# Optimization experiments

Hardware: AMD Instinct MI355X
Metric: run time of the kernel (lower is better)

The kernel has to match this reference:

```python
import jax, jax.numpy as jnp
import numpy as np

B, C, H, W = 8, 256, 64, 64
NH = 8            # num_heads
OC = 256          # out_channels
D = C // NH       # per-head channel dim = 32
HW = H * W
BN_EPS = 1e-5


def _conv1x1(x, Wt, b):
    # x: [B,Cin,H,W], Wt: [Cout,Cin]
    return jnp.einsum('bchw,oc->bohw', x, Wt) + b[None, :, None, None]


def setup_inputs() -> dict:
    key = jax.random.key(0)
    ks = jax.random.split(key, 16)
    def n(k, shape, s=0.05):
        return jax.random.normal(k, shape, dtype=jnp.float32) * s
    return {
        'F1': jax.random.normal(ks[0], (B, C, H, W), jnp.float32),
        'F2': jax.random.normal(ks[1], (B, C, H, W), jnp.float32),
        'Wq':  n(ks[2], (C, 2 * C)), 'bq':  n(ks[3], (C,)),
        'Wk1': n(ks[4], (C, C)),     'bk1': n(ks[5], (C,)),
        'Wv1': n(ks[6], (C, C)),     'bv1': n(ks[7], (C,)),
        'Wk2': n(ks[8], (C, C)),     'bk2': n(ks[9], (C,)),
        'Wv2': n(ks[10], (C, C)),    'bv2': n(ks[11], (C,)),
        'mu':  jnp.full((1,), 0.5, jnp.float32),   # learnable scalar (init 0 in torch; nonzero here for nontrivial math)
        'Wc':  n(ks[12], (OC, 2 * C, 3, 3)),
        'gamma': jnp.ones((OC,), jnp.float32),
        'beta':  jnp.zeros((OC,), jnp.float32),
        'rmean': jnp.zeros((OC,), jnp.float32),
        'rvar':  jnp.ones((OC,), jnp.float32),
    }


def reference(F1, F2, Wq, bq, Wk1, bk1, Wv1, bv1, Wk2, bk2, Wv2, bv2,
              mu, Wc, gamma, beta, rmean, rvar):
    # fused query from both streams
    Qf = _conv1x1(jnp.concatenate([F1, F2], axis=1), Wq, bq)          # [B,C,H,W]
    Q = Qf.reshape(B, NH, D, HW).transpose(0, 1, 3, 2)                # [B,h,HW,d]
    Qs = jax.nn.softmax(Q, axis=-1)                                   # softmax over d

    def branch(F, Wk, bk, Wv, bv):
        K = _conv1x1(F, Wk, bk).reshape(B, NH, D, HW)                 # [B,h,d,HW]
        V = _conv1x1(F, Wv, bv).reshape(B, NH, D, HW)                 # [B,h,d,HW]
        Ks = jax.nn.softmax(K, axis=-1)                               # softmax over HW
        Att = jnp.einsum('bhdn,bhne->bhde', Ks, Qs)                   # [B,h,d,d]
        Xw = jnp.einsum('bhde,bhen->bhdn', Att, V)                    # [B,h,d,HW]
        return Xw.reshape(B, C, H, W)

    X1 = branch(F1, Wk1, bk1, Wv1, bv1)
    X2 = branch(F2, Wk2, bk2, Wv2, bv2)

    fused = jnp.concatenate([mu * X1 + F1, mu * X2 + F2], axis=1)     # [B,2C,H,W]
    y = jax.lax.conv_general_dilated(
        fused, Wc, window_strides=(1, 1), padding='SAME',
        dimension_numbers=('NCHW', 'OIHW', 'NCHW'))                   # [B,OC,H,W]
    # inference-mode BatchNorm + ReLU
    inv = gamma / jnp.sqrt(rvar + BN_EPS)
    y = y * inv[None, :, None, None] + (beta - rmean * inv)[None, :, None, None]
    return jax.nn.relu(y)
```

## Files before the change

### kernel.cpp

```cpp
#include <hip/hip_runtime.h>

typedef __attribute__((ext_vector_type(8))) short bf8;
typedef __attribute__((ext_vector_type(4))) float f32x4;

static __device__ __forceinline__ unsigned short f2b(float x) {
    unsigned u = __builtin_bit_cast(unsigned, x);
    u += 0x7fffu + ((u >> 16) & 1u);
    return (unsigned short)(u >> 16);
}

static __device__ __forceinline__ void gload_lds16(const void* g, void* l) {
    __builtin_amdgcn_global_load_lds(
        (const __attribute__((address_space(1))) unsigned int*)g,
        (__attribute__((address_space(3))) unsigned int*)l, 16, 0, 0);
}

__global__ __launch_bounds__(256) void k_prep_w(
    const float* __restrict__ Wq, const float* __restrict__ Wk1, const float* __restrict__ Wv1,
    const float* __restrict__ Wk2, const float* __restrict__ Wv2, const float* __restrict__ Wc,
    const float* __restrict__ gamma, const float* __restrict__ beta,
    const float* __restrict__ rmean, const float* __restrict__ rvar,
    unsigned short* __restrict__ WQB, unsigned short* __restrict__ WK1B, unsigned short* __restrict__ WV1B,
    unsigned short* __restrict__ WK2B, unsigned short* __restrict__ WV2B, unsigned short* __restrict__ WCB,
    float* __restrict__ BNS, float* __restrict__ BNB)
{
    const int total = 131072 + 4 * 65536 + 1179648 + 256;
    for (int i = blockIdx.x * blockDim.x + threadIdx.x; i < total; i += gridDim.x * blockDim.x) {
        int j = i;
        if (j < 131072) { WQB[j] = f2b(Wq[j]); continue; }
        j -= 131072;
        if (j < 65536) { WK1B[j] = f2b(Wk1[j]); continue; }
        j -= 65536;
        if (j < 65536) { WV1B[j] = f2b(Wv1[j]); continue; }
        j -= 65536;
        if (j < 65536) { WK2B[j] = f2b(Wk2[j]); continue; }
        j -= 65536;
        if (j < 65536) { WV2B[j] = f2b(Wv2[j]); continue; }
        j -= 65536;
        if (j < 1179648) {
            int cl = j & 63;
            int rest = j >> 6;
            int o = rest & 255;
            int tc = rest >> 8;
            int tap = tc >> 3, ccb = tc & 7;
            int c = ccb * 64 + cl;
            WCB[j] = f2b(Wc[(size_t)(o * 512 + c) * 9 + tap]);
            continue;
        }
        j -= 1179648;
        float inv = gamma[j] * rsqrtf(rvar[j] + 1e-5f);
        BNS[j] = inv;
        BNB[j] = beta[j] - rmean[j] * inv;
    }
}

__global__ __launch_bounds__(256) void k_xt(const float* __restrict__ F1, const float* __restrict__ F2,
                                            unsigned short* __restrict__ XT)
{
    __shared__ float tile[64][65];
    const int b = blockIdx.z;
    const int c0 = blockIdx.y * 64;
    const int p0 = blockIdx.x * 64;
    const int tx = threadIdx.x & 63;
    const int ty = threadIdx.x >> 6;
    const float* src = (c0 < 256) ? F1 : F2;
    const int cb = c0 & 255;
#pragma unroll
    for (int i = 0; i < 16; i++) {
        int cl = i * 4 + ty;
        tile[cl][tx] = src[((size_t)b * 256 + cb + cl) * 4096 + p0 + tx];
    }
    __syncthreads();
    const int t = threadIdx.x;
    const int p = t >> 2;
    const int cg = (t & 3) * 16;
    unsigned short tmp[16];
#pragma unroll
    for (int j = 0; j < 16; j++) tmp[j] = f2b(tile[cg + j][p]);
    unsigned short* dst = XT + ((size_t)b * 4096 + p0 + p) * 512 + c0 + cg;
    *(uint4*)dst = *(const uint4*)tmp;
    *(uint4*)(dst + 8) = *(const uint4*)(tmp + 8);
}

template<int MODE>
__global__ __launch_bounds__(256) void k_gemm1x1(
    const unsigned short* __restrict__ A,
    const unsigned short* __restrict__ XT,
    const float* __restrict__ bias,
    unsigned short* __restrict__ outU,
    float* __restrict__ outF,
    const unsigned short* __restrict__ QSp,
    float* __restrict__ ATTP,
    int Kd, int coff)
{
    __shared__ unsigned short lds[2][2][128 * 64];
    const int b = blockIdx.z;
    const int m0 = blockIdx.y * 128;
    const int n0 = blockIdx.x * 128;
    const int lane = threadIdx.x & 63;
    const int wv = threadIdx.x >> 6;
    const int wr = wv >> 1, wc = wv & 1;
    const int lrow = lane & 15, kg = lane >> 4;
    const int px = lane >> 3, sl = lane & 7;
    const int nt = Kd >> 6;

    f32x4 acc[4][4];
#pragma unroll
    for (int mi = 0; mi < 4; mi++)
#pragma unroll
        for (int ni = 0; ni < 4; ni++)
            acc[mi][ni] = (f32x4){0.f, 0.f, 0.f, 0.f};

#pragma unroll
    for (int j = 0; j < 4; j++) {
        int r0 = wv * 32 + j * 8;
        gload_lds16(A + (size_t)(m0 + r0 + px) * Kd + (sl ^ px) * 8, &lds[0][0][r0 * 64]);
        gload_lds16(XT + ((size_t)b * 4096 + n0 + r0 + px) * 512 + coff + (sl ^ px) * 8, &lds[0][1][r0 * 64]);
    }
    __syncthreads();

    int cb = 0;
    for (int kt = 0; kt < nt; kt++) {
        if (kt + 1 < nt) {
            int k0 = (kt + 1) << 6;
            int nb = cb ^ 1;
#pragma unroll
            for (int j = 0; j < 4; j++) {
                int r0 = wv * 32 + j * 8;
                gload_lds16(A + (size_t)(m0 + r0 + px) * Kd + k0 + (sl ^ px) * 8, &lds[nb][0][r0 * 64]);
                gload_lds16(XT + ((size_t)b * 4096 + n0 + r0 + px) * 512 + coff + k0 + (sl ^ px) * 8, &lds[nb][1][r0 * 64]);
            }
        }
        const unsigned short* wa = lds[cb][0];
        const unsigned short* wb = lds[cb][1];
#pragma unroll
        for (int klo = 0; klo < 64; klo += 32) {
            const int slin = klo >> 3;
            bf8 a[4], bv[4];
#pragma unroll
            for (int mi = 0; mi < 4; mi++) {
                int ol = wr * 64 + mi * 16 + lrow;
                a[mi] = *(const bf8*)(wa + ol * 64 + (((slin + kg) ^ (ol & 7)) * 8));
            }
#pragma unroll
            for (int ni = 0; ni < 4; ni++) {
                int nl = wc * 64 + ni * 16 + lrow;
                bv[ni] = *(const bf8*)(wb + nl * 64 + (((slin + kg) ^ (nl & 7)) * 8));
            }
#pragma unroll
            for (int mi = 0; mi < 4; mi++)
#pragma unroll
                for (int ni = 0; ni < 4; ni++)
                    acc[mi][ni] = __builtin_amdgcn_mfma_f32_16x16x32_bf16(a[mi], bv[ni], acc[mi][ni], 0, 0, 0);
        }
        __syncthreads();
        cb ^= 1;
    }

    if (MODE == 1) {
#pragma unroll
        for (int mi = 0; mi < 4; mi++) {
#pragma unroll
            for (int ni = 0; ni < 4; ni++) {
                int row0 = m0 + wr * 64 + mi * 16 + kg * 4;
                int col = n0 + wc * 64 + ni * 16 + lrow;
                int h = row0 >> 5, e0 = row0 & 31;
                unsigned long long pk = 0;
#pragma unroll
                for (int r = 0; r < 4; r++) {
                    unsigned short us = f2b(acc[mi][ni][r] + bias[row0 + r]);
                    pk |= (unsigned long long)us << (16 * r);
                }
                *(unsigned long long*)(outU + (((size_t)b * 8 + h) * 4096 + col) * 32 + e0) = pk;
            }
        }
    } else if (MODE == 2) {
#pragma unroll
        for (int hh = 0; hh < 2; hh++) {
            float vv[2][4][4];
            float mx[4];
#pragma unroll
            for (int ni = 0; ni < 4; ni++) mx[ni] = -1e30f;
#pragma unroll
            for (int ms = 0; ms < 2; ms++) {
                int mi = hh * 2 + ms;
                int row0 = m0 + wr * 64 + mi * 16 + kg * 4;
#pragma unroll
                for (int r = 0; r < 4; r++) {
                    float bi = bias[row0 + r];
#pragma unroll
                    for (int ni = 0; ni < 4; ni++) {
                        float x = acc[mi][ni][r] + bi;
                        vv[ms][r][ni] = x;
                        mx[ni] = fmaxf(mx[ni], x);
                    }
                }
            }
#pragma unroll
            for (int ni = 0; ni < 4; ni++) {
                mx[ni] = fmaxf(mx[ni], __shfl_xor(mx[ni], 16, 64));
                mx[ni] = fmaxf(mx[ni], __shfl_xor(mx[ni], 32, 64));
            }
            float sm[4] = {0.f, 0.f, 0.f, 0.f};
#pragma unroll
            for (int ms = 0; ms < 2; ms++)
#pragma unroll
                for (int r = 0; r < 4; r++)
#pragma unroll
                    for (int ni = 0; ni < 4; ni++) {
                        float e = __expf(vv[ms][r][ni] - mx[ni]);
                        vv[ms][r][ni] = e;
                        sm[ni] += e;
                    }
#pragma unroll
            for (int ni = 0; ni < 4; ni++) {
                sm[ni] += __shfl_xor(sm[ni], 16, 64);
                sm[ni] += __shfl_xor(sm[ni], 32, 64);
                sm[ni] = 1.0f / sm[ni];
            }
            int h = (m0 + wr * 64 + hh * 32) >> 5;
#pragma unroll
            for (int ms = 0; ms < 2; ms++) {
                int e0 = ms * 16 + kg * 4;
#pragma unroll
                for (int r = 0; r < 4; r++)
#pragma unroll
                    for (int ni = 0; ni < 4; ni++) {
                        int col = n0 + wc * 64 + ni * 16 + lrow;
                        outU[((size_t)(b * 8 + h) * 32 + e0 + r) * 4096 + col] = f2b(vv[ms][r][ni] * sm[ni]);
                    }
            }
        }
    } else {
        unsigned short* P = &lds[0][0][0];
        float* red = (float*)&lds[1][0][0];
        float ps[4][4];
#pragma unroll
        for (int mi = 0; mi < 4; mi++) {
            int rowl0 = wr * 64 + mi * 16 + kg * 4;
#pragma unroll
            for (int r = 0; r < 4; r++) {
                float bi = bias[m0 + rowl0 + r];
                int row = rowl0 + r;
                float s = 0.f;
#pragma unroll
                for (int ni = 0; ni < 4; ni++) {
                    float e = __expf(acc[mi][ni][r] + bi);
                    int col = wc * 64 + ni * 16 + lrow;
                    int slot = (col >> 3) ^ (row & 7);
                    P[row * 128 + slot * 8 + (col & 7)] = f2b(e);
                    s += e;
                }
                ps[mi][r] = s;
            }
        }
#pragma unroll
        for (int mi = 0; mi < 4; mi++)
#pragma unroll
            for (int r = 0; r < 4; r++)
                red[(wr * 64 + mi * 16 + kg * 4 + r) * 33 + wc * 16 + lrow] = ps[mi][r];
        __syncthreads();
        if (threadIdx.x < 128) {
            float s = 0.f;
#pragma unroll
            for (int j = 0; j < 32; j++) s += red[threadIdx.x * 33 + j];
            atomicAdd(&outF[b * 256 + m0 + threadIdx.x], s);
        }
        const int hh = wv;
        const int bh = b * 8 + (m0 >> 5) + hh;
        const unsigned short* QSb = QSp + ((size_t)bh * 32) * 4096 + n0;
        f32x4 acc2[2][2];
#pragma unroll
        for (int mi2 = 0; mi2 < 2; mi2++)
#pragma unroll
            for (int ni2 = 0; ni2 < 2; ni2++)
                acc2[mi2][ni2] = (f32x4){0.f, 0.f, 0.f, 0.f};
#pragma unroll
        for (int ks = 0; ks < 4; ks++) {
            bf8 pa[2], qb[2];
#pragma unroll
            for (int mi2 = 0; mi2 < 2; mi2++) {
                int row = hh * 32 + mi2 * 16 + lrow;
                int slot = (ks * 4 + kg) ^ (row & 7);
                pa[mi2] = *(const bf8*)(P + row * 128 + slot * 8);
            }
#pragma unroll
            for (int ni2 = 0; ni2 < 2; ni2++)
                qb[ni2] = *(const bf8*)(QSb + (size_t)(ni2 * 16 + lrow) * 4096 + ks * 32 + kg * 8);
#pragma unroll
            for (int mi2 = 0; mi2 < 2; mi2++)
#pragma unroll
                for (int ni2 = 0; ni2 < 2; ni2++)
                    acc2[mi2][ni2] = __builtin_amdgcn_mfma_f32_16x16x32_bf16(pa[mi2], qb[ni2], acc2[mi2][ni2], 0, 0, 0);
        }
        float* dst = ATTP + ((size_t)bh * 32 + (n0 >> 7)) * 1024;
#pragma unroll
        for (int mi2 = 0; mi2 < 2; mi2++)
#pragma unroll
            for (int ni2 = 0; ni2 < 2; ni2++)
#pragma unroll
                for (int r = 0; r < 4; r++)
                    dst[(mi2 * 16 + kg * 4 + r) * 32 + ni2 * 16 + lrow] = acc2[mi2][ni2][r];
    }
}

__global__ __launch_bounds__(256) void k_att_red(const float* __restrict__ ATTP,
                                                 const float* __restrict__ SUMK,
                                                 const float* __restrict__ mup,
                                                 unsigned short* __restrict__ ATT)
{
    const int bh = blockIdx.x;
    const int b = bh >> 3, h = bh & 7;
    const int tid = threadIdx.x;
    const float mu = mup[0];
#pragma unroll
    for (int i = 0; i < 4; i++) {
        int idx = tid + i * 256;
        int d = idx >> 5;
        float s = 0.f;
        for (int nch = 0; nch < 32; nch++)
            s += ATTP[((size_t)bh * 32 + nch) * 1024 + idx];
        ATT[(size_t)bh * 1024 + idx] = f2b(mu * s / SUMK[b * 256 + h * 32 + d]);
    }
}

__global__ __launch_bounds__(256) void k_xw(
    const unsigned short* __restrict__ ATT1, const unsigned short* __restrict__ ATT2,
    const unsigned short* __restrict__ V1T, const unsigned short* __restrict__ V2T,
    unsigned short* __restrict__ FUSED)
{
    const int pt = blockIdx.x, h = blockIdx.y;
    const int bz = blockIdx.z;
    const int br = bz >> 3, b = bz & 7;
    const unsigned short* ATT = br ? ATT2 : ATT1;
    const unsigned short* VT = br ? V2T : V1T;
    const int cofs = br * 256;
    const int lane = threadIdx.x & 63, wave = threadIdx.x >> 6;
    const int lrow = lane & 15, kg = lane >> 4;
    const int n0 = pt * 128 + wave * 32;
    const int bh = b * 8 + h;

    const unsigned short* Apt = ATT + (size_t)bh * 1024;
    const unsigned short* Bpt = VT + ((size_t)bh * 4096 + n0 + lrow) * 32 + kg * 8;

    bf8 a[2], bb[2];
#pragma unroll
    for (int mi = 0; mi < 2; mi++)
        a[mi] = *(const bf8*)(Apt + (mi * 16 + lrow) * 32 + kg * 8);
#pragma unroll
    for (int ni = 0; ni < 2; ni++)
        bb[ni] = *(const bf8*)(Bpt + ni * 16 * 32);

    f32x4 acc[2][2];
#pragma unroll
    for (int mi = 0; mi < 2; mi++)
#pragma unroll
        for (int ni = 0; ni < 2; ni++)
            acc[mi][ni] = (f32x4){0.f, 0.f, 0.f, 0.f};
#pragma unroll
    for (int mi = 0; mi < 2; mi++)
#pragma unroll
        for (int ni = 0; ni < 2; ni++)
            acc[mi][ni] = __builtin_amdgcn_mfma_f32_16x16x32_bf16(a[mi], bb[ni], acc[mi][ni], 0, 0, 0);

#pragma unroll
    for (int mi = 0; mi < 2; mi++) {
#pragma unroll
        for (int ni = 0; ni < 2; ni++) {
            int d0 = mi * 16 + kg * 4;
            int p = n0 + ni * 16 + lrow;
            unsigned short* addr = FUSED + ((size_t)b * 4096 + p) * 512 + cofs + h * 32 + d0;
            unsigned long long rin = *(const unsigned long long*)addr;
            unsigned long long pk = 0;
#pragma unroll
            for (int r = 0; r < 4; r++) {
                unsigned short us = (unsigned short)(rin >> (16 * r));
                float f = __builtin_bit_cast(float, ((unsigned)us) << 16);
                float x = acc[mi][ni][r] + f;
                pk |= (unsigned long long)f2b(x) << (16 * r);
            }
            *(unsigned long long*)addr = pk;
        }
    }
}

__global__ __launch_bounds__(256) void k_conv3(
    const unsigned short* __restrict__ WB2,
    const unsigned short* __restrict__ FUSED,
    const float* __restrict__ BNS, const float* __restrict__ BNB,
    float* __restrict__ out)
{
    __shared__ unsigned short lds_in[4 * 72 * 64];
    __shared__ unsigned short lds_w[2][128 * 64];

    const int b = blockIdx.z;
    const int m0 = blockIdx.y * 128;
    const int ry = blockIdx.x;
    const int lane = threadIdx.x & 63;
    const int wv = threadIdx.x >> 6;
    const int wr = wv >> 1, wc = wv & 1;
    const int lrow = lane & 15, kg = lane >> 4;
    const int px = lane >> 3, sl = lane & 7;

    f32x4 acc[4][4];
#pragma unroll
    for (int mi = 0; mi < 4; mi++)
#pragma unroll
        for (int ni = 0; ni < 4; ni++)
            acc[mi][ni] = (f32x4){0.f, 0.f, 0.f, 0.f};

    for (int ccb = 0; ccb < 8; ccb++) {
        for (int u = wv; u < 36; u += 4) {
            int rl = u / 9, seg = u - rl * 9;
            int gy = ry * 2 + rl - 1;
            bool rowok = ((unsigned)gy < 64u);
            int xi0 = seg * 8;
            unsigned short* ldsb = lds_in + (rl * 72 + xi0) * 64;
            int x = xi0 + px - 4;
            const unsigned short* src = FUSED
                + ((size_t)(b * 4096 + gy * 64 + x)) * 512 + ccb * 64 + (sl ^ px) * 8;
            if (rowok && seg >= 1 && seg <= 7) {
                gload_lds16(src, ldsb);
            } else {
                uint4 v = {0u, 0u, 0u, 0u};
                if (rowok && ((unsigned)x < 64u)) v = *(const uint4*)src;
                *(uint4*)(ldsb + lane * 8) = v;
            }
        }
        {
            const unsigned short* base = WB2 + (((size_t)(0 * 8 + ccb) * 256) + m0) * 64;
#pragma unroll
            for (int j = 0; j < 4; j++) {
                int o0 = wv * 32 + j * 8;
                gload_lds16(base + (size_t)(o0 + px) * 64 + (sl ^ px) * 8, &lds_w[0][o0 * 64]);
            }
        }
        __syncthreads();

        for (int tap = 0; tap < 9; tap++) {
            if (tap < 8) {
                const unsigned short* base = WB2 + (((size_t)((tap + 1) * 8 + ccb) * 256) + m0) * 64;
                unsigned short* wdst = lds_w[(tap + 1) & 1];
#pragma unroll
                for (int j = 0; j < 4; j++) {
                    int o0 = wv * 32 + j * 8;
                    gload_lds16(base + (size_t)(o0 + px) * 64 + (sl ^ px) * 8, &wdst[o0 * 64]);
                }
            }
            const unsigned short* wb = lds_w[tap & 1];
            const int ky = tap / 3, kx = tap - ky * 3;
            const int rl = wc + ky;
#pragma unroll
            for (int k0 = 0; k0 < 64; k0 += 32) {
                const int slin = k0 >> 3;
                bf8 a[4], bv[4];
#pragma unroll
                for (int mi = 0; mi < 4; mi++) {
                    int ol = wr * 64 + mi * 16 + lrow;
                    int s = (slin + kg) ^ (ol & 7);
                    a[mi] = *(const bf8*)(wb + ol * 64 + s * 8);
                }
#pragma unroll
                for (int ni = 0; ni < 4; ni++) {
                    int xi = ni * 16 + lrow + kx + 3;
                    int s = (slin + kg) ^ (xi & 7);
                    bv[ni] = *(const bf8*)(lds_in + (rl * 72 + xi) * 64 + s * 8);
                }
#pragma unroll
                for (int mi = 0; mi < 4; mi++)
#pragma unroll
                    for (int ni = 0; ni < 4; ni++)
                        acc[mi][ni] = __builtin_amdgcn_mfma_f32_16x16x32_bf16(a[mi], bv[ni], acc[mi][ni], 0, 0, 0);
            }
            __syncthreads();
        }
    }

#pragma unroll
    for (int mi = 0; mi < 4; mi++) {
#pragma unroll
        for (int ni = 0; ni < 4; ni++) {
            int o0 = m0 + wr * 64 + mi * 16 + kg * 4;
            int p = (ry * 2 + wc) * 64 + ni * 16 + lrow;
#pragma unroll
            for (int r = 0; r < 4; r++) {
                int o = o0 + r;
                float v = acc[mi][ni][r] * BNS[o] + BNB[o];
                out[((size_t)b * 256 + o) * 4096 + p] = fmaxf(v, 0.0f);
            }
        }
    }
}

extern "C" void kernel_launch(void* const* d_in, const int* in_sizes, int n_in,
                              void* d_out, int out_size, void* d_ws, size_t ws_size,
                              hipStream_t stream)
{
    (void)in_sizes; (void)n_in; (void)out_size; (void)ws_size;
    const float* F1 = (const float*)d_in[0];
    const float* F2 = (const float*)d_in[1];
    const float* Wq = (const float*)d_in[2];
    const float* bq = (const float*)d_in[3];
    const float* Wk1 = (const float*)d_in[4];
    const float* bk1 = (const float*)d_in[5];
    const float* Wv1 = (const float*)d_in[6];
    const float* bv1 = (const float*)d_in[7];
    const float* Wk2 = (const float*)d_in[8];
    const float* bk2 = (const float*)d_in[9];
    const float* Wv2 = (const float*)d_in[10];
    const float* bv2 = (const float*)d_in[11];
    const float* mu = (const float*)d_in[12];
    const float* Wc = (const float*)d_in[13];
    const float* gamma = (const float*)d_in[14];
    const float* beta = (const float*)d_in[15];
    const float* rmean = (const float*)d_in[16];
    const float* rvar = (const float*)d_in[17];

    char* ws = (char*)d_ws;
    size_t off = 0;
    auto give = [&](size_t bytes) -> char* {
        char* p = ws + off;
        off = (off + bytes + 255) & ~(size_t)255;
        return p;
    };
    unsigned short* XT  = (unsigned short*)give(33554432);
    unsigned short* QS  = (unsigned short*)give(16777216);
    unsigned short* V1T = (unsigned short*)give(16777216);
    unsigned short* V2T = (unsigned short*)give(16777216);
    unsigned short* WQB  = (unsigned short*)give(262144);
    unsigned short* WK1B = (unsigned short*)give(131072);
    unsigned short* WV1B = (unsigned short*)give(131072);
    unsigned short* WK2B = (unsigned short*)give(131072);
    unsigned short* WV2B = (unsigned short*)give(131072);
    unsigned short* WCB  = (unsigned short*)give(2359296);
    unsigned short* ATT1 = (unsigned short*)give(131072);
    unsigned short* ATT2 = (unsigned short*)give(131072);
    float* BNS = (float*)give(1024);
    float* BNB = (float*)give(1024);
    float* ATTP = (float*)give(8388608);
    float* SUMK = (float*)give(16384);
    unsigned short* FUSED = XT;
    float* SUMK1 = SUMK, *SUMK2 = SUMK + 2048;

    hipMemsetAsync(SUMK, 0, 16384, stream);
    k_prep_w<<<1024, 256, 0, stream>>>(Wq, Wk1, Wv1, Wk2, Wv2, Wc, gamma, beta, rmean, rvar,
                                       WQB, WK1B, WV1B, WK2B, WV2B, WCB, BNS, BNB);
    k_xt<<<dim3(64, 8, 8), 256, 0, stream>>>(F1, F2, XT);

    k_gemm1x1<2><<<dim3(32, 2, 8), 256, 0, stream>>>(WQB, XT, bq, QS, nullptr, nullptr, nullptr, 512, 0);

    k_gemm1x1<3><<<dim3(32, 2, 8), 256, 0, stream>>>(WK1B, XT, bk1, nullptr, SUMK1, QS, ATTP, 256, 0);
    k_gemm1x1<1><<<dim3(32, 2, 8), 256, 0, stream>>>(WV1B, XT, bv1, V1T, nullptr, nullptr, nullptr, 256, 0);
    k_att_red<<<64, 256, 0, stream>>>(ATTP, SUMK1, mu, ATT1);

    k_gemm1x1<3><<<dim3(32, 2, 8), 256, 0, stream>>>(WK2B, XT, bk2, nullptr, SUMK2, QS, ATTP, 256, 256);
    k_gemm1x1<1><<<dim3(32, 2, 8), 256, 0, stream>>>(WV2B, XT, bv2, V2T, nullptr, nullptr, nullptr, 256, 256);
    k_att_red<<<64, 256, 0, stream>>>(ATTP, SUMK2, mu, ATT2);

    k_xw<<<dim3(32, 8, 16), 256, 0, stream>>>(ATT1, ATT2, V1T, V2T, FUSED);

    k_conv3<<<dim3(32, 2, 8), 256, 0, stream>>>(WCB, FUSED, BNS, BNB, (float*)d_out);
}
```

Baseline: 206.1 us.

## Fuse attention-times-V into value GEMM epilogue and restage conv3 weights in registers

```diff
diff --git a/kernel.cpp b/kernel.cpp
--- a/kernel.cpp
+++ b/kernel.cpp
@@ -157,24 +157,7 @@
         cb ^= 1;
     }
 
-    if (MODE == 1) {
-#pragma unroll
-        for (int mi = 0; mi < 4; mi++) {
-#pragma unroll
-            for (int ni = 0; ni < 4; ni++) {
-                int row0 = m0 + wr * 64 + mi * 16 + kg * 4;
-                int col = n0 + wc * 64 + ni * 16 + lrow;
-                int h = row0 >> 5, e0 = row0 & 31;
-                unsigned long long pk = 0;
-#pragma unroll
-                for (int r = 0; r < 4; r++) {
-                    unsigned short us = f2b(acc[mi][ni][r] + bias[row0 + r]);
-                    pk |= (unsigned long long)us << (16 * r);
-                }
-                *(unsigned long long*)(outU + (((size_t)b * 8 + h) * 4096 + col) * 32 + e0) = pk;
-            }
-        }
-    } else if (MODE == 2) {
+    if (MODE == 2) {
 #pragma unroll
         for (int hh = 0; hh < 2; hh++) {
             float vv[2][4][4];
@@ -231,7 +214,7 @@
                     }
             }
         }
-    } else {
+    } else if (MODE == 3) {
         unsigned short* P = &lds[0][0][0];
         float* red = (float*)&lds[1][0][0];
         float ps[4][4];
@@ -301,6 +284,56 @@
 #pragma unroll
                 for (int r = 0; r < 4; r++)
                     dst[(mi2 * 16 + kg * 4 + r) * 32 + ni2 * 16 + lrow] = acc2[mi2][ni2][r];
+    } else {
+        unsigned short* vlds = &lds[0][0][0];
+#pragma unroll
+        for (int mi = 0; mi < 4; mi++) {
+#pragma unroll
+            for (int ni = 0; ni < 4; ni++) {
+                int ch0 = wr * 64 + mi * 16 + kg * 4;
+                int p = wc * 64 + ni * 16 + lrow;
+                int sg = ch0 >> 3;
+                unsigned long long pk = 0;
+#pragma unroll
+                for (int r = 0; r < 4; r++) {
+                    unsigned short us = f2b(acc[mi][ni][r] + bias[m0 + ch0 + r]);
+                    pk |= (unsigned long long)us << (16 * r);
+                }
+                *(unsigned long long*)(vlds + p * 128 + ((sg ^ (p & 15)) * 8) + (ch0 & 7)) = pk;
+            }
+        }
+        __syncthreads();
+        const int hl = wv;
+        const int bh = b * 8 + (m0 >> 5) + hl;
+        const unsigned short* ATTh = QSp + (size_t)bh * 1024;
+        bf8 af[2];
+#pragma unroll
+        for (int mi2 = 0; mi2 < 2; mi2++)
+            af[mi2] = *(const bf8*)(ATTh + (mi2 * 16 + lrow) * 32 + kg * 8);
+#pragma unroll
+        for (int ni2 = 0; ni2 < 8; ni2++) {
+            int pp = ni2 * 16 + lrow;
+            bf8 bf = *(const bf8*)(vlds + pp * 128 + (((hl * 4 + kg) ^ (pp & 15)) * 8));
+            f32x4 pa0 = (f32x4){0.f, 0.f, 0.f, 0.f};
+            f32x4 pa1 = (f32x4){0.f, 0.f, 0.f, 0.f};
+            pa0 = __builtin_amdgcn_mfma_f32_16x16x32_bf16(af[0], bf, pa0, 0, 0, 0);
+            pa1 = __builtin_amdgcn_mfma_f32_16x16x32_bf16(af[1], bf, pa1, 0, 0, 0);
+#pragma unroll
+            for (int mi2 = 0; mi2 < 2; mi2++) {
+                f32x4 pa = mi2 ? pa1 : pa0;
+                int c0 = coff + m0 + hl * 32 + mi2 * 16 + kg * 4;
+                size_t base = ((size_t)b * 4096 + n0 + pp) * 512 + c0;
+                unsigned long long rin = *(const unsigned long long*)(XT + base);
+                unsigned long long pk = 0;
+#pragma unroll
+                for (int r = 0; r < 4; r++) {
+                    unsigned short us = (unsigned short)(rin >> (16 * r));
+                    float f = __builtin_bit_cast(float, ((unsigned)us) << 16);
+                    pk |= (unsigned long long)f2b(pa[r] + f) << (16 * r);
+                }
+                *(unsigned long long*)(outU + base) = pk;
+            }
+        }
     }
 }
 
@@ -324,84 +357,50 @@
     }
 }
 
-__global__ __launch_bounds__(256) void k_xw(
-    const unsigned short* __restrict__ ATT1, const unsigned short* __restrict__ ATT2,
-    const unsigned short* __restrict__ V1T, const unsigned short* __restrict__ V2T,
-    unsigned short* __restrict__ FUSED)
-{
-    const int pt = blockIdx.x, h = blockIdx.y;
-    const int bz = blockIdx.z;
-    const int br = bz >> 3, b = bz & 7;
-    const unsigned short* ATT = br ? ATT2 : ATT1;
-    const unsigned short* VT = br ? V2T : V1T;
-    const int cofs = br * 256;
-    const int lane = threadIdx.x & 63, wave = threadIdx.x >> 6;
-    const int lrow = lane & 15, kg = lane >> 4;
-    const int n0 = pt * 128 + wave * 32;
-    const int bh = b * 8 + h;
-
-    const unsigned short* Apt = ATT + (size_t)bh * 1024;
-    const unsigned short* Bpt = VT + ((size_t)bh * 4096 + n0 + lrow) * 32 + kg * 8;
-
-    bf8 a[2], bb[2];
-#pragma unroll
-    for (int mi = 0; mi < 2; mi++)
-        a[mi] = *(const bf8*)(Apt + (mi * 16 + lrow) * 32 + kg * 8);
-#pragma unroll
-    for (int ni = 0; ni < 2; ni++)
-        bb[ni] = *(const bf8*)(Bpt + ni * 16 * 32);
-
-    f32x4 acc[2][2];
-#pragma unroll
-    for (int mi = 0; mi < 2; mi++)
-#pragma unroll
-        for (int ni = 0; ni < 2; ni++)
-            acc[mi][ni] = (f32x4){0.f, 0.f, 0.f, 0.f};
-#pragma unroll
-    for (int mi = 0; mi < 2; mi++)
-#pragma unroll
-        for (int ni = 0; ni < 2; ni++)
-            acc[mi][ni] = __builtin_amdgcn_mfma_f32_16x16x32_bf16(a[mi], bb[ni], acc[mi][ni], 0, 0, 0);
-
-#pragma unroll
-    for (int mi = 0; mi < 2; mi++) {
-#pragma unroll
-        for (int ni = 0; ni < 2; ni++) {
-            int d0 = mi * 16 + kg * 4;
-            int p = n0 + ni * 16 + lrow;
-            unsigned short* addr = FUSED + ((size_t)b * 4096 + p) * 512 + cofs + h * 32 + d0;
-            unsigned long long rin = *(const unsigned long long*)addr;
-            unsigned long long pk = 0;
-#pragma unroll
-            for (int r = 0; r < 4; r++) {
-                unsigned short us = (unsigned short)(rin >> (16 * r));
-                float f = __builtin_bit_cast(float, ((unsigned)us) << 16);
-                float x = acc[mi][ni][r] + f;
-                pk |= (unsigned long long)f2b(x) << (16 * r);
-            }
-            *(unsigned long long*)addr = pk;
-        }
-    }
-}
-
 __global__ __launch_bounds__(256) void k_conv3(
     const unsigned short* __restrict__ WB2,
     const unsigned short* __restrict__ FUSED,
     const float* __restrict__ BNS, const float* __restrict__ BNB,
     float* __restrict__ out)
 {
-    __shared__ unsigned short lds_in[4 * 72 * 64];
-    __shared__ unsigned short lds_w[2][128 * 64];
+    __shared__ unsigned short halo[4 * 72 * 64];
 
     const int b = blockIdx.z;
     const int m0 = blockIdx.y * 128;
     const int ry = blockIdx.x;
-    const int lane = threadIdx.x & 63;
-    const int wv = threadIdx.x >> 6;
+    const int tid = threadIdx.x;
+    const int lane = tid & 63;
+    const int wv = tid >> 6;
     const int wr = wv >> 1, wc = wv & 1;
     const int lrow = lane & 15, kg = lane >> 4;
     const int px = lane >> 3, sl = lane & 7;
 
+    {
+        const uint4 z = {0u, 0u, 0u, 0u};
+        int r = tid >> 6, l = tid & 63;
+        int xig = l >> 3;
+        int xi = xig < 4 ? xig : 64 + xig;
+        *(uint4*)(halo + (r * 72 + xi) * 64 + (l & 7) * 8) = z;
+        if (ry == 0) {
+            for (int j = tid; j < 576; j += 256) *(uint4*)(halo + j * 8) = z;
+        } else if (ry == 31) {
+            for (int j = tid; j < 576; j += 256) *(uint4*)(halo + 3 * 72 * 64 + j * 8) = z;
+        }
+    }
+
+    auto stage_halo = [&](int ccb) {
+        for (int u = wv; u < 32; u += 4) {
+            int rl = u >> 3, seg = u & 7;
+            int gy = ry * 2 + rl - 1;
+            if ((unsigned)gy < 64u) {
+                int x = seg * 8 + px;
+                int slot = sl ^ ((x + 4) & 7);
+                gload_lds16(FUSED + ((size_t)(b * 4096 + gy * 64 + x)) * 512 + ccb * 64 + slot * 8,
+                            halo + (rl * 72 + seg * 8 + 4) * 64);
+            }
+        }
+    };
+
     f32x4 acc[4][4];
 #pragma unroll
     for (int mi = 0; mi < 4; mi++)
@@ -409,69 +408,48 @@
         for (int ni = 0; ni < 4; ni++)
             acc[mi][ni] = (f32x4){0.f, 0.f, 0.f, 0.f};
 
+    bf8 acur[8], anxt[8];
+    auto LDA = [&](bf8* dst, int tap, int ccb) {
+#pragma unroll
+        for (int q = 0; q < 8; q++) {
+            int ks = q >> 2, mi = q & 3;
+            dst[q] = *(const bf8*)(WB2 + (((size_t)(tap * 8 + ccb) * 256) + m0 + wr * 64 + mi * 16 + lrow) * 64
+                                   + (ks * 4 + kg) * 8);
+        }
+    };
+
+    stage_halo(0);
+    LDA(acur, 0, 0);
+    __syncthreads();
+
     for (int ccb = 0; ccb < 8; ccb++) {
-        for (int u = wv; u < 36; u += 4) {
-            int rl = u / 9, seg = u - rl * 9;
-            int gy = ry * 2 + rl - 1;
-            bool rowok = ((unsigned)gy < 64u);
-            int xi0 = seg * 8;
-            unsigned short* ldsb = lds_in + (rl * 72 + xi0) * 64;
-            int x = xi0 + px - 4;
-            const unsigned short* src = FUSED
-                + ((size_t)(b * 4096 + gy * 64 + x)) * 512 + ccb * 64 + (sl ^ px) * 8;
-            if (rowok && seg >= 1 && seg <= 7) {
-                gload_lds16(src, ldsb);
-            } else {
-                uint4 v = {0u, 0u, 0u, 0u};
-                if (rowok && ((unsigned)x < 64u)) v = *(const uint4*)src;
-                *(uint4*)(ldsb + lane * 8) = v;
-            }
-        }
-        {
-            const unsigned short* base = WB2 + (((size_t)(0 * 8 + ccb) * 256) + m0) * 64;
-#pragma unroll
-            for (int j = 0; j < 4; j++) {
-                int o0 = wv * 32 + j * 8;
-                gload_lds16(base + (size_t)(o0 + px) * 64 + (sl ^ px) * 8, &lds_w[0][o0 * 64]);
-            }
-        }
-        __syncthreads();
-
+#pragma unroll
         for (int tap = 0; tap < 9; tap++) {
-            if (tap < 8) {
-                const unsigned short* base = WB2 + (((size_t)((tap + 1) * 8 + ccb) * 256) + m0) * 64;
-                unsigned short* wdst = lds_w[(tap + 1) & 1];
-#pragma unroll
-                for (int j = 0; j < 4; j++) {
-                    int o0 = wv * 32 + j * 8;
-                    gload_lds16(base + (size_t)(o0 + px) * 64 + (sl ^ px) * 8, &wdst[o0 * 64]);
-                }
-            }
-            const unsigned short* wb = lds_w[tap & 1];
+            if (tap < 8) LDA(anxt, tap + 1, ccb);
+            else LDA(anxt, 0, ccb < 7 ? ccb + 1 : 0);
             const int ky = tap / 3, kx = tap - ky * 3;
             const int rl = wc + ky;
 #pragma unroll
-            for (int k0 = 0; k0 < 64; k0 += 32) {
-                const int slin = k0 >> 3;
-                bf8 a[4], bv[4];
-#pragma unroll
-                for (int mi = 0; mi < 4; mi++) {
-                    int ol = wr * 64 + mi * 16 + lrow;
-                    int s = (slin + kg) ^ (ol & 7);
-                    a[mi] = *(const bf8*)(wb + ol * 64 + s * 8);
-                }
+            for (int ks = 0; ks < 2; ks++) {
+                bf8 bv[4];
 #pragma unroll
                 for (int ni = 0; ni < 4; ni++) {
                     int xi = ni * 16 + lrow + kx + 3;
-                    int s = (slin + kg) ^ (xi & 7);
-                    bv[ni] = *(const bf8*)(lds_in + (rl * 72 + xi) * 64 + s * 8);
+                    int s = (ks * 4 + kg) ^ (xi & 7);
+                    bv[ni] = *(const bf8*)(halo + (rl * 72 + xi) * 64 + s * 8);
                 }
 #pragma unroll
                 for (int mi = 0; mi < 4; mi++)
 #pragma unroll
                     for (int ni = 0; ni < 4; ni++)
-                        acc[mi][ni] = __builtin_amdgcn_mfma_f32_16x16x32_bf16(a[mi], bv[ni], acc[mi][ni], 0, 0, 0);
-            }
+                        acc[mi][ni] = __builtin_amdgcn_mfma_f32_16x16x32_bf16(acur[ks * 4 + mi], bv[ni], acc[mi][ni], 0, 0, 0);
+            }
+#pragma unroll
+            for (int q = 0; q < 8; q++) acur[q] = anxt[q];
+        }
+        if (ccb < 7) {
+            __syncthreads();
+            stage_halo(ccb + 1);
             __syncthreads();
         }
     }
@@ -523,10 +501,9 @@
         off = (off + bytes + 255) & ~(size_t)255;
         return p;
     };
-    unsigned short* XT  = (unsigned short*)give(33554432);
+    unsigned short* XT     = (unsigned short*)give(33554432);
+    unsigned short* FUSED2 = (unsigned short*)give(33554432);
     unsigned short* QS  = (unsigned short*)give(16777216);
-    unsigned short* V1T = (unsigned short*)give(16777216);
-    unsigned short* V2T = (unsigned short*)give(16777216);
     unsigned short* WQB  = (unsigned short*)give(262144);
     unsigned short* WK1B = (unsigned short*)give(131072);
     unsigned short* WV1B = (unsigned short*)give(131072);
@@ -539,7 +516,6 @@
     float* BNB = (float*)give(1024);
     float* ATTP = (float*)give(8388608);
     float* SUMK = (float*)give(16384);
-    unsigned short* FUSED = XT;
     float* SUMK1 = SUMK, *SUMK2 = SUMK + 2048;
 
     hipMemsetAsync(SUMK, 0, 16384, stream);
@@ -550,14 +526,12 @@
     k_gemm1x1<2><<<dim3(32, 2, 8), 256, 0, stream>>>(WQB, XT, bq, QS, nullptr, nullptr, nullptr, 512, 0);
 
     k_gemm1x1<3><<<dim3(32, 2, 8), 256, 0, stream>>>(WK1B, XT, bk1, nullptr, SUMK1, QS, ATTP, 256, 0);
-    k_gemm1x1<1><<<dim3(32, 2, 8), 256, 0, stream>>>(WV1B, XT, bv1, V1T, nullptr, nullptr, nullptr, 256, 0);
     k_att_red<<<64, 256, 0, stream>>>(ATTP, SUMK1, mu, ATT1);
+    k_gemm1x1<4><<<dim3(32, 2, 8), 256, 0, stream>>>(WV1B, XT, bv1, FUSED2, nullptr, ATT1, nullptr, 256, 0);
 
     k_gemm1x1<3><<<dim3(32, 2, 8), 256, 0, stream>>>(WK2B, XT, bk2, nullptr, SUMK2, QS, ATTP, 256, 256);
-    k_gemm1x1<1><<<dim3(32, 2, 8), 256, 0, stream>>>(WV2B, XT, bv2, V2T, nullptr, nullptr, nullptr, 256, 256);
     k_att_red<<<64, 256, 0, stream>>>(ATTP, SUMK2, mu, ATT2);
-
-    k_xw<<<dim3(32, 8, 16), 256, 0, stream>>>(ATT1, ATT2, V1T, V2T, FUSED);
-
-    k_conv3<<<dim3(32, 2, 8), 256, 0, stream>>>(WCB, FUSED, BNS, BNB, (float*)d_out);
-}
+    k_gemm1x1<4><<<dim3(32, 2, 8), 256, 0, stream>>>(WV2B, XT, bv2, FUSED2, nullptr, ATT2, nullptr, 256, 256);
+
+    k_conv3<<<dim3(32, 2, 8), 256, 0, stream>>>(WCB, FUSED2, BNS, BNB, (float*)d_out);
+}
```

Result: slower. 308.4 us (+49.6%).
